# Optimization experiments

Hardware: AMD Instinct MI355X
Metric: run time of the kernel (lower is better)

## Reference

```python
import jax, jax.numpy as jnp
import numpy as np

EPS = 1e-7  # entropy eps
DIAG_EPS = 1e-8
LEAK = 0.2  # LeakyReLU slope


def _entropy(p):
    # EntropyLoss: mean over leading dims of -sum(p*log(p+eps), -1)
    return jnp.mean(-jnp.sum(p * jnp.log(p + EPS), axis=-1))


def setup_inputs() -> dict:
    key = jax.random.key(0)
    ks = jax.random.split(key, 7)
    B, S, C, F, E, H = 256, 6, 80, 2048, 300, 1024
    x = jax.random.normal(ks[0], (B, F, 14, 14), dtype=jnp.float32)
    inp = jax.random.normal(ks[1], (C, E), dtype=jnp.float32) * 0.1
    y = (jax.random.uniform(ks[2], (B, C)) < 0.1).astype(jnp.float32)
    # persistent co-occurrence buffer (non-negative counts)
    comatrix = jax.random.uniform(ks[3], (S, C, C), dtype=jnp.float32) * 50.0
    W_scene = jax.random.normal(ks[4], (F, S), dtype=jnp.float32) * 0.02
    W1 = jax.random.uniform(ks[5], (E, H), dtype=jnp.float32, minval=-1, maxval=1) / np.sqrt(H)
    W2 = jax.random.uniform(ks[6], (H, F), dtype=jnp.float32, minval=-1, maxval=1) / np.sqrt(F)
    return {"x": x, "inp": inp, "y": y, "comatrix": comatrix,
            "W_scene": W_scene, "W1": W1, "W2": W2}


def reference(x, inp, y, comatrix, W_scene, W1, W2):
    B = x.shape[0]
    S, C, _ = comatrix.shape
    # backbone output -> MaxPool2d(14,14) == global max over the 14x14 map
    img_feats = jnp.max(x, axis=(2, 3))                       # [B, F]
    scene_scores = img_feats @ W_scene                        # [B, S]
    scene_probs = jax.nn.softmax(scene_scores, axis=-1)
    # --- training-path comatrix scatter update (comat_smooth=False) ---
    batch_comats = y[:, :, None] * y[:, None, :]              # [B, C, C]
    ids = jnp.argmax(scene_probs, axis=-1)                    # [B]
    comatrix = comatrix + jnp.zeros_like(comatrix).at[ids].add(batch_comats)
    # --- entropy terms ---
    sample_en = _entropy(scene_probs)
    max_en = _entropy(jnp.full((S,), 1.0 / S, dtype=scene_probs.dtype))
    batch_en = (max_en - _entropy(jnp.mean(scene_probs, axis=0))) * 100.0
    # --- comatrix2prob: row-normalize by diagonal, force diag=1 ---
    diag = jnp.diagonal(comatrix, axis1=1, axis2=2)[:, :, None]  # [S, C, 1]
    comat = comatrix / (diag + DIAG_EPS)
    eye = jnp.eye(C, dtype=comat.dtype)
    comat = comat * (1.0 - eye) + eye
    comats = comat[ids]                                       # gather [B, C, C]
    # --- gen_adj: adj = D^{-1/2} A^T D^{-1/2}, D = rowsums(A) ---
    D = jax.lax.rsqrt(jnp.sum(comats, axis=2))                # [B, C]
    adjs = D[:, :, None] * jnp.swapaxes(comats, 1, 2) * D[:, None, :]
    # --- 2-layer GCN ---
    h = adjs @ (inp @ W1)                                     # [B, C, 1024]
    h = jnp.where(h > 0, h, LEAK * h)
    h = adjs @ (h @ W2)                                       # [B, C, 2048]
    output = jnp.einsum('bcf,bf->bc', h, img_feats)           # [B, C]
    return (output, scene_probs, sample_en, batch_en, comats)
```

## Files before the change

kernel.cpp:

```cpp
#include <hip/hip_runtime.h>
#include <math.h>

#define B_ 256
#define S_ 6
#define C_ 80
#define F_ 2048
#define E_ 300
#define H_ 1024
#define EPS_ 1e-7f
#define DEPS_ 1e-8f
#define LEAK_ 0.2f

#define IMG_OFF   0u
#define Z_OFF     524288u
#define COMAT_OFF 606208u
#define ADJA_OFF  644608u
#define G_OFF     683008u
#define G2_OFF    1174528u
#define PART_OFF  1666048u
#define IDS_OFF   5860352u
#define MP_OFF    5860608u
#define SEN_OFF   5860614u

#define OUT0_OFF 0
#define PROB_OFF 20480
#define SEN_OUT  22016
#define BEN_OUT  22017
#define CMTS_OFF 22018

__global__ __launch_bounds__(256) void k_maxpool(const float* __restrict__ x,
                                                 float* __restrict__ img) {
    int pair = blockIdx.x * 4 + (threadIdx.x >> 6);
    int lane = threadIdx.x & 63;
    const float4* xp = (const float4*)x + (size_t)pair * 49;
    float m = -INFINITY;
    if (lane < 49) {
        float4 v = xp[lane];
        m = fmaxf(fmaxf(v.x, v.y), fmaxf(v.z, v.w));
    }
#pragma unroll
    for (int off = 32; off >= 1; off >>= 1) m = fmaxf(m, __shfl_xor(m, off));
    if (lane == 0) img[pair] = m;
}

__global__ __launch_bounds__(256) void k_scene(const float* __restrict__ img,
                                               const float* __restrict__ Ws,
                                               float* __restrict__ probs_out,
                                               int* __restrict__ ids,
                                               float* __restrict__ mp,
                                               float* __restrict__ sen) {
    __shared__ float red[6][256];
    int b = blockIdx.x, tid = threadIdx.x;
    float acc[6] = {0, 0, 0, 0, 0, 0};
#pragma unroll
    for (int i = 0; i < 8; i++) {
        int f = tid + i * 256;
        float a = img[b * F_ + f];
#pragma unroll
        for (int s = 0; s < 6; s++) acc[s] += a * Ws[f * 6 + s];
    }
    for (int s = 0; s < 6; s++) red[s][tid] = acc[s];
    __syncthreads();
    for (int off = 128; off > 0; off >>= 1) {
        if (tid < off)
            for (int s = 0; s < 6; s++) red[s][tid] += red[s][tid + off];
        __syncthreads();
    }
    if (tid == 0) {
        float sc[6], mx = -INFINITY;
        for (int s = 0; s < 6; s++) { sc[s] = red[s][0]; mx = fmaxf(mx, sc[s]); }
        float sum = 0.f;
        for (int s = 0; s < 6; s++) { sc[s] = expf(sc[s] - mx); sum += sc[s]; }
        float inv = 1.0f / sum;
        float p[6], ent = 0.f;
        int best = 0; float bv = -1.f;
        for (int s = 0; s < 6; s++) {
            p[s] = sc[s] * inv;
            probs_out[b * 6 + s] = p[s];
            ent -= p[s] * logf(p[s] + EPS_);
            if (p[s] > bv) { bv = p[s]; best = s; }
            atomicAdd(&mp[s], p[s]);
        }
        atomicAdd(sen, ent);
        ids[b] = best;
    }
}

__global__ __launch_bounds__(256) void k_comat(const float* __restrict__ y,
                                               const float* __restrict__ cm_in,
                                               const int* __restrict__ ids,
                                               float* __restrict__ comat,
                                               float* __restrict__ adjA) {
    int s = blockIdx.x, tid = threadIdx.x;
    __shared__ unsigned long long colq[80][4];
    __shared__ float cm[6400];
    __shared__ float diag[80], Dn[80];
    __shared__ int idsL[256];
    idsL[tid] = ids[tid];
    __syncthreads();
    int wave = tid >> 6, lane = tid & 63;
    int b = tid;
    bool ok = (idsL[b] == s);
    for (int i = 0; i < 80; i++) {
        bool pred = ok && (y[b * 80 + i] != 0.0f);
        unsigned long long mk = __ballot(pred);
        if (lane == 0) colq[i][wave] = mk;
    }
    __syncthreads();
    for (int p = tid; p < 6400; p += 256) {
        int i = p / 80, j = p - i * 80;
        int cnt = 0;
#pragma unroll
        for (int w = 0; w < 4; w++) cnt += __popcll(colq[i][w] & colq[j][w]);
        cm[p] = cm_in[s * 6400 + p] + (float)cnt;
    }
    __syncthreads();
    if (tid < 80) diag[tid] = cm[tid * 81];
    __syncthreads();
    for (int p = tid; p < 6400; p += 256) {
        int i = p / 80, j = p - i * 80;
        float v = (i == j) ? 1.0f : cm[p] / (diag[i] + DEPS_);
        cm[p] = v;
        comat[s * 6400 + p] = v;
    }
    __syncthreads();
    if (tid < 80) {
        float rs = 0.f;
        for (int j = 0; j < 80; j++) rs += cm[tid * 80 + j];
        Dn[tid] = 1.0f / sqrtf(rs);
    }
    __syncthreads();
    for (int p = tid; p < 6400; p += 256) {
        int i = p / 80, j = p - i * 80;
        adjA[s * 6400 + p] = Dn[i] * cm[j * 80 + i] * Dn[j];
    }
}

__global__ __launch_bounds__(256) void k_z(const float* __restrict__ inp,
                                           const float* __restrict__ W1,
                                           float* __restrict__ Z) {
    int c = blockIdx.x >> 2;
    int h = ((blockIdx.x & 3) << 8) + threadIdx.x;
    float acc = 0.f;
    for (int e = 0; e < E_; e++) acc += inp[c * E_ + e] * W1[e * H_ + h];
    Z[c * H_ + h] = acc;
}

__global__ __launch_bounds__(256) void k_g(const float* __restrict__ adjA,
                                           const float* __restrict__ Z,
                                           float* __restrict__ g) {
    int s = blockIdx.x / 80, c = blockIdx.x % 80;
    const float* row = adjA + (s * 80 + c) * 80;
    const float4* Z4 = (const float4*)Z;
    float4 acc = {0, 0, 0, 0};
    for (int j = 0; j < 80; j++) {
        float a = row[j];
        float4 z = Z4[j * 256 + threadIdx.x];
        acc.x += a * z.x; acc.y += a * z.y; acc.z += a * z.z; acc.w += a * z.w;
    }
    acc.x = acc.x > 0.f ? acc.x : LEAK_ * acc.x;
    acc.y = acc.y > 0.f ? acc.y : LEAK_ * acc.y;
    acc.z = acc.z > 0.f ? acc.z : LEAK_ * acc.z;
    acc.w = acc.w > 0.f ? acc.w : LEAK_ * acc.w;
    ((float4*)g)[(s * 80 + c) * 256 + threadIdx.x] = acc;
}

__global__ __launch_bounds__(256) void k_g2(const float* __restrict__ adjA,
                                            const float* __restrict__ g,
                                            float* __restrict__ G2) {
    int s = blockIdx.x / 80, c = blockIdx.x % 80;
    const float* row = adjA + (s * 80 + c) * 80;
    const float4* g4 = (const float4*)(g + (size_t)s * 80 * 1024);
    float4 acc = {0, 0, 0, 0};
    for (int j = 0; j < 80; j++) {
        float a = row[j];
        float4 z = g4[j * 256 + threadIdx.x];
        acc.x += a * z.x; acc.y += a * z.y; acc.z += a * z.z; acc.w += a * z.w;
    }
    ((float4*)G2)[(s * 80 + c) * 256 + threadIdx.x] = acc;
}

__global__ __launch_bounds__(256) void k_ugemm(const float* __restrict__ A,
                                               const float* __restrict__ Bm,
                                               float* __restrict__ part) {
    __shared__ float As[16 * 68];
    __shared__ float Bs[16 * 132];
    int tid = threadIdx.x;
    int m0 = blockIdx.y * 64, h0 = blockIdx.x * 128;
    int kbase = blockIdx.z * 128;
    float acc[4][8];
#pragma unroll
    for (int i = 0; i < 4; i++)
#pragma unroll
        for (int j = 0; j < 8; j++) acc[i][j] = 0.f;
    int r0 = (tid >> 4) << 2, c0 = (tid & 15) << 3;
    for (int st = 0; st < 8; st++) {
        int kc = kbase + st * 16;
        {
            int r = tid >> 2, kq = tid & 3;
            float4 av = *(const float4*)(A + (size_t)(m0 + r) * 2048 + kc + (kq << 2));
            int kk = kq << 2;
            As[(kk + 0) * 68 + r] = av.x; As[(kk + 1) * 68 + r] = av.y;
            As[(kk + 2) * 68 + r] = av.z; As[(kk + 3) * 68 + r] = av.w;
        }
#pragma unroll
        for (int l = 0; l < 2; l++) {
            int fid = tid + (l << 8);
            int r = fid >> 2, kq = fid & 3;
            float4 bv = *(const float4*)(Bm + (size_t)(h0 + r) * 2048 + kc + (kq << 2));
            int kk = kq << 2;
            Bs[(kk + 0) * 132 + r] = bv.x; Bs[(kk + 1) * 132 + r] = bv.y;
            Bs[(kk + 2) * 132 + r] = bv.z; Bs[(kk + 3) * 132 + r] = bv.w;
        }
        __syncthreads();
#pragma unroll
        for (int k = 0; k < 16; k++) {
            float4 a0 = *(const float4*)&As[k * 68 + r0];
            float4 b0 = *(const float4*)&Bs[k * 132 + c0];
            float4 b1 = *(const float4*)&Bs[k * 132 + c0 + 4];
            float ar[4] = {a0.x, a0.y, a0.z, a0.w};
            float br[8] = {b0.x, b0.y, b0.z, b0.w, b1.x, b1.y, b1.z, b1.w};
#pragma unroll
            for (int i = 0; i < 4; i++)
#pragma unroll
                for (int j = 0; j < 8; j++) acc[i][j] += ar[i] * br[j];
        }
        __syncthreads();
    }
    float* pu = part + (size_t)blockIdx.z * 262144;
#pragma unroll
    for (int i = 0; i < 4; i++) {
        int row = m0 + r0 + i;
        float4 v0 = {acc[i][0], acc[i][1], acc[i][2], acc[i][3]};
        float4 v1 = {acc[i][4], acc[i][5], acc[i][6], acc[i][7]};
        *(float4*)(pu + (size_t)row * 1024 + h0 + c0) = v0;
        *(float4*)(pu + (size_t)row * 1024 + h0 + c0 + 4) = v1;
    }
}

__global__ __launch_bounds__(256) void k_out(const float* __restrict__ part,
                                             const float* __restrict__ G2,
                                             const int* __restrict__ ids,
                                             float* __restrict__ out0) {
    __shared__ float ul[1024];
    int b = blockIdx.x, tid = threadIdx.x;
    int s = ids[b];
    for (int h = tid; h < 1024; h += 256) {
        float a = 0.f;
#pragma unroll
        for (int z = 0; z < 16; z++) a += part[z * 262144 + b * 1024 + h];
        ul[h] = a;
    }
    __syncthreads();
    int wave = tid >> 6, lane = tid & 63;
    const float4* u4 = (const float4*)ul;
    for (int c = wave; c < 80; c += 4) {
        const float4* row = (const float4*)(G2 + (size_t)(s * 80 + c) * 1024);
        float a = 0.f;
#pragma unroll
        for (int t = 0; t < 4; t++) {
            float4 gv = row[lane + t * 64];
            float4 uv = u4[lane + t * 64];
            a += gv.x * uv.x + gv.y * uv.y + gv.z * uv.z + gv.w * uv.w;
        }
#pragma unroll
        for (int off = 32; off >= 1; off >>= 1) a += __shfl_xor(a, off);
        if (lane == 0) out0[b * 80 + c] = a;
    }
}

__global__ __launch_bounds__(256) void k_gather(const float* __restrict__ comat,
                                                const int* __restrict__ ids,
                                                float* __restrict__ cmts) {
    int b = blockIdx.x;
    int s = ids[b];
    const float2* src = (const float2*)(comat + s * 6400);
    float2* dst = (float2*)(cmts + (size_t)b * 6400);
    for (int i = threadIdx.x; i < 3200; i += 256) dst[i] = src[i];
}

__global__ void k_final(const float* __restrict__ mp, const float* __restrict__ sen,
                        float* __restrict__ o_sen, float* __restrict__ o_ben) {
    if (threadIdx.x == 0 && blockIdx.x == 0) {
        *o_sen = *sen / 256.0f;
        float ent = 0.f;
        for (int s = 0; s < 6; s++) {
            float q = mp[s] / 256.0f;
            ent -= q * logf(q + EPS_);
        }
        float invS = 1.0f / 6.0f;
        float men = -6.0f * (invS * logf(invS + EPS_));
        *o_ben = (men - ent) * 100.0f;
    }
}

extern "C" void kernel_launch(void* const* d_in, const int* in_sizes, int n_in,
                              void* d_out, int out_size, void* d_ws, size_t ws_size,
                              hipStream_t stream) {
    const float* x    = (const float*)d_in[0];
    const float* inp  = (const float*)d_in[1];
    const float* y    = (const float*)d_in[2];
    const float* cmin = (const float*)d_in[3];
    const float* Ws   = (const float*)d_in[4];
    const float* W1   = (const float*)d_in[5];
    const float* W2   = (const float*)d_in[6];
    float* out = (float*)d_out;
    float* W = (float*)d_ws;

    float* img   = W + IMG_OFF;
    float* Z     = W + Z_OFF;
    float* comat = W + COMAT_OFF;
    float* adjA  = W + ADJA_OFF;
    float* g     = W + G_OFF;
    float* G2    = W + G2_OFF;
    float* part  = W + PART_OFF;
    int*   ids   = (int*)(W + IDS_OFF);
    float* mp    = W + MP_OFF;
    float* sen   = W + SEN_OFF;

    hipMemsetAsync(mp, 0, 7 * sizeof(float), stream);
    k_maxpool<<<131072, 256, 0, stream>>>(x, img);
    k_scene<<<256, 256, 0, stream>>>(img, Ws, out + PROB_OFF, ids, mp, sen);
    k_comat<<<6, 256, 0, stream>>>(y, cmin, ids, comat, adjA);
    k_z<<<320, 256, 0, stream>>>(inp, W1, Z);
    k_g<<<480, 256, 0, stream>>>(adjA, Z, g);
    k_g2<<<480, 256, 0, stream>>>(adjA, g, G2);
    k_ugemm<<<dim3(8, 4, 16), 256, 0, stream>>>(img, W2, part);
    k_out<<<256, 256, 0, stream>>>(part, G2, ids, out + OUT0_OFF);
    k_gather<<<256, 256, 0, stream>>>(comat, ids, out + CMTS_OFF);
    k_final<<<1, 64, 0, stream>>>(mp, sen, out + SEN_OUT, out + BEN_OUT);
}
```

Measured before the change: 678.2 us.

## Fuse GCN layers in LDS, merge gather/final into other kernels, restructure maxpool

Merges the two adjacency-multiply kernels into one that holds the adjacency and a 64-column slice of Z and of the intermediate in shared memory, so the intermediate g never goes to global memory. The gather of comats moves into k_out and the scalar entropy finalisation moves into k_comat, which removes two launches. Maxpool now handles 16 feature maps per block through shared memory instead of one wave per map. The fused GCN kernel launches only 96 blocks, which may leave much of the GPU idle, and the new maxpool adds shared-memory round trips to the largest memory-bound stage.

```diff
diff --git a/kernel.cpp b/kernel.cpp
--- a/kernel.cpp
+++ b/kernel.cpp
@@ -15,12 +15,11 @@
 #define Z_OFF     524288u
 #define COMAT_OFF 606208u
 #define ADJA_OFF  644608u
-#define G_OFF     683008u
-#define G2_OFF    1174528u
-#define PART_OFF  1666048u
-#define IDS_OFF   5860352u
-#define MP_OFF    5860608u
-#define SEN_OFF   5860614u
+#define G2_OFF    683008u
+#define PART_OFF  1174528u
+#define IDS_OFF   5368832u
+#define MP_OFF    5369088u
+#define SEN_OFF   5369094u
 
 #define OUT0_OFF 0
 #define PROB_OFF 20480
@@ -30,17 +29,27 @@
 
 __global__ __launch_bounds__(256) void k_maxpool(const float* __restrict__ x,
                                                  float* __restrict__ img) {
-    int pair = blockIdx.x * 4 + (threadIdx.x >> 6);
-    int lane = threadIdx.x & 63;
-    const float4* xp = (const float4*)x + (size_t)pair * 49;
-    float m = -INFINITY;
-    if (lane < 49) {
-        float4 v = xp[lane];
-        m = fmaxf(fmaxf(v.x, v.y), fmaxf(v.z, v.w));
-    }
-#pragma unroll
-    for (int off = 32; off >= 1; off >>= 1) m = fmaxf(m, __shfl_xor(m, off));
-    if (lane == 0) img[pair] = m;
+    __shared__ float m1[784];
+    __shared__ float m2[16][17];
+    int tid = threadIdx.x;
+    const float4* base = (const float4*)x + (size_t)blockIdx.x * 784;
+    for (int i = tid; i < 784; i += 256) {
+        float4 v = base[i];
+        m1[i] = fmaxf(fmaxf(v.x, v.y), fmaxf(v.z, v.w));
+    }
+    __syncthreads();
+    int p = tid >> 4, i = tid & 15;
+    int o = p * 49 + i;
+    float a = fmaxf(m1[o], fmaxf(m1[o + 16], m1[o + 32]));
+    if (i == 0) a = fmaxf(a, m1[p * 49 + 48]);
+    m2[p][i] = a;
+    __syncthreads();
+    if (tid < 16) {
+        float r = m2[tid][0];
+#pragma unroll
+        for (int j = 1; j < 16; j++) r = fmaxf(r, m2[tid][j]);
+        img[blockIdx.x * 16 + tid] = r;
+    }
 }
 
 __global__ __launch_bounds__(256) void k_scene(const float* __restrict__ img,
@@ -89,9 +98,24 @@
 __global__ __launch_bounds__(256) void k_comat(const float* __restrict__ y,
                                                const float* __restrict__ cm_in,
                                                const int* __restrict__ ids,
+                                               const float* __restrict__ mp,
+                                               const float* __restrict__ sen,
                                                float* __restrict__ comat,
-                                               float* __restrict__ adjA) {
+                                               float* __restrict__ adjA,
+                                               float* __restrict__ o_sen,
+                                               float* __restrict__ o_ben) {
     int s = blockIdx.x, tid = threadIdx.x;
+    if (s == 0 && tid == 0) {
+        *o_sen = *sen / 256.0f;
+        float ent = 0.f;
+        for (int q = 0; q < 6; q++) {
+            float v = mp[q] / 256.0f;
+            ent -= v * logf(v + EPS_);
+        }
+        float invS = 1.0f / 6.0f;
+        float men = -6.0f * (invS * logf(invS + EPS_));
+        *o_ben = (men - ent) * 100.0f;
+    }
     __shared__ unsigned long long colq[80][4];
     __shared__ float cm[6400];
     __shared__ float diag[80], Dn[80];
@@ -99,10 +123,9 @@
     idsL[tid] = ids[tid];
     __syncthreads();
     int wave = tid >> 6, lane = tid & 63;
-    int b = tid;
-    bool ok = (idsL[b] == s);
+    bool ok = (idsL[tid] == s);
     for (int i = 0; i < 80; i++) {
-        bool pred = ok && (y[b * 80 + i] != 0.0f);
+        bool pred = ok && (y[tid * 80 + i] != 0.0f);
         unsigned long long mk = __ballot(pred);
         if (lane == 0) colq[i][wave] = mk;
     }
@@ -146,38 +169,34 @@
     Z[c * H_ + h] = acc;
 }
 
-__global__ __launch_bounds__(256) void k_g(const float* __restrict__ adjA,
-                                           const float* __restrict__ Z,
-                                           float* __restrict__ g) {
-    int s = blockIdx.x / 80, c = blockIdx.x % 80;
-    const float* row = adjA + (s * 80 + c) * 80;
-    const float4* Z4 = (const float4*)Z;
-    float4 acc = {0, 0, 0, 0};
-    for (int j = 0; j < 80; j++) {
-        float a = row[j];
-        float4 z = Z4[j * 256 + threadIdx.x];
-        acc.x += a * z.x; acc.y += a * z.y; acc.z += a * z.z; acc.w += a * z.w;
-    }
-    acc.x = acc.x > 0.f ? acc.x : LEAK_ * acc.x;
-    acc.y = acc.y > 0.f ? acc.y : LEAK_ * acc.y;
-    acc.z = acc.z > 0.f ? acc.z : LEAK_ * acc.z;
-    acc.w = acc.w > 0.f ? acc.w : LEAK_ * acc.w;
-    ((float4*)g)[(s * 80 + c) * 256 + threadIdx.x] = acc;
-}
-
-__global__ __launch_bounds__(256) void k_g2(const float* __restrict__ adjA,
-                                            const float* __restrict__ g,
-                                            float* __restrict__ G2) {
-    int s = blockIdx.x / 80, c = blockIdx.x % 80;
-    const float* row = adjA + (s * 80 + c) * 80;
-    const float4* g4 = (const float4*)(g + (size_t)s * 80 * 1024);
-    float4 acc = {0, 0, 0, 0};
-    for (int j = 0; j < 80; j++) {
-        float a = row[j];
-        float4 z = g4[j * 256 + threadIdx.x];
-        acc.x += a * z.x; acc.y += a * z.y; acc.z += a * z.z; acc.w += a * z.w;
-    }
-    ((float4*)G2)[(s * 80 + c) * 256 + threadIdx.x] = acc;
+__global__ __launch_bounds__(256) void k_gg2(const float* __restrict__ adjA,
+                                             const float* __restrict__ Z,
+                                             float* __restrict__ G2) {
+    __shared__ float aL[6400];
+    __shared__ float zL[80 * 64];
+    __shared__ float gL[80 * 64];
+    int s = blockIdx.x >> 4;
+    int c0 = (blockIdx.x & 15) << 6;
+    int tid = threadIdx.x;
+    int c = tid & 63, r4 = tid >> 6;
+    for (int p = tid; p < 6400; p += 256) aL[p] = adjA[s * 6400 + p];
+    for (int j = r4; j < 80; j += 4) zL[j * 64 + c] = Z[j * 1024 + c0 + c];
+    __syncthreads();
+    for (int pass = 0; pass < 20; pass++) {
+        int r = pass * 4 + r4;
+        float acc = 0.f;
+#pragma unroll 8
+        for (int j = 0; j < 80; j++) acc += aL[r * 80 + j] * zL[j * 64 + c];
+        gL[r * 64 + c] = acc > 0.f ? acc : LEAK_ * acc;
+    }
+    __syncthreads();
+    for (int pass = 0; pass < 20; pass++) {
+        int r = pass * 4 + r4;
+        float acc = 0.f;
+#pragma unroll 8
+        for (int j = 0; j < 80; j++) acc += aL[r * 80 + j] * gL[j * 64 + c];
+        G2[(size_t)(s * 80 + r) * 1024 + c0 + c] = acc;
+    }
 }
 
 __global__ __launch_bounds__(256) void k_ugemm(const float* __restrict__ A,
@@ -240,8 +259,10 @@
 
 __global__ __launch_bounds__(256) void k_out(const float* __restrict__ part,
                                              const float* __restrict__ G2,
+                                             const float* __restrict__ comat,
                                              const int* __restrict__ ids,
-                                             float* __restrict__ out0) {
+                                             float* __restrict__ out0,
+                                             float* __restrict__ cmts) {
     __shared__ float ul[1024];
     int b = blockIdx.x, tid = threadIdx.x;
     int s = ids[b];
@@ -267,31 +288,9 @@
         for (int off = 32; off >= 1; off >>= 1) a += __shfl_xor(a, off);
         if (lane == 0) out0[b * 80 + c] = a;
     }
-}
-
-__global__ __launch_bounds__(256) void k_gather(const float* __restrict__ comat,
-                                                const int* __restrict__ ids,
-                                                float* __restrict__ cmts) {
-    int b = blockIdx.x;
-    int s = ids[b];
-    const float2* src = (const float2*)(comat + s * 6400);
-    float2* dst = (float2*)(cmts + (size_t)b * 6400);
-    for (int i = threadIdx.x; i < 3200; i += 256) dst[i] = src[i];
-}
-
-__global__ void k_final(const float* __restrict__ mp, const float* __restrict__ sen,
-                        float* __restrict__ o_sen, float* __restrict__ o_ben) {
-    if (threadIdx.x == 0 && blockIdx.x == 0) {
-        *o_sen = *sen / 256.0f;
-        float ent = 0.f;
-        for (int s = 0; s < 6; s++) {
-            float q = mp[s] / 256.0f;
-            ent -= q * logf(q + EPS_);
-        }
-        float invS = 1.0f / 6.0f;
-        float men = -6.0f * (invS * logf(invS + EPS_));
-        *o_ben = (men - ent) * 100.0f;
-    }
+    const float4* src = (const float4*)(comat + s * 6400);
+    float4* dst = (float4*)(cmts + (size_t)b * 6400);
+    for (int i = tid; i < 1600; i += 256) dst[i] = src[i];
 }
 
 extern "C" void kernel_launch(void* const* d_in, const int* in_sizes, int n_in,
@@ -311,7 +310,6 @@
     float* Z     = W + Z_OFF;
     float* comat = W + COMAT_OFF;
     float* adjA  = W + ADJA_OFF;
-    float* g     = W + G_OFF;
     float* G2    = W + G2_OFF;
     float* part  = W + PART_OFF;
     int*   ids   = (int*)(W + IDS_OFF);
@@ -319,14 +317,13 @@
     float* sen   = W + SEN_OFF;
 
     hipMemsetAsync(mp, 0, 7 * sizeof(float), stream);
-    k_maxpool<<<131072, 256, 0, stream>>>(x, img);
+    k_maxpool<<<32768, 256, 0, stream>>>(x, img);
     k_scene<<<256, 256, 0, stream>>>(img, Ws, out + PROB_OFF, ids, mp, sen);
-    k_comat<<<6, 256, 0, stream>>>(y, cmin, ids, comat, adjA);
+    k_comat<<<6, 256, 0, stream>>>(y, cmin, ids, mp, sen, comat, adjA,
+                                   out + SEN_OUT, out + BEN_OUT);
     k_z<<<320, 256, 0, stream>>>(inp, W1, Z);
-    k_g<<<480, 256, 0, stream>>>(adjA, Z, g);
-    k_g2<<<480, 256, 0, stream>>>(adjA, g, G2);
+    k_gg2<<<96, 256, 0, stream>>>(adjA, Z, G2);
     k_ugemm<<<dim3(8, 4, 16), 256, 0, stream>>>(img, W2, part);
-    k_out<<<256, 256, 0, stream>>>(part, G2, ids, out + OUT0_OFF);
-    k_gather<<<256, 256, 0, stream>>>(comat, ids, out + CMTS_OFF);
-    k_final<<<1, 64, 0, stream>>>(mp, sen, out + SEN_OUT, out + BEN_OUT);
-}
+    k_out<<<256, 256, 0, stream>>>(part, G2, comat, ids,
+                                   out + OUT0_OFF, out + CMTS_OFF);
+}
```

Measured after the change: 688.8 us. Within noise of the previous version (+1.6%).
